# Kernel optimization log

Measured on AMD Instinct MI355X. Metric: run time of the kernel, lower is better.

The kernel has to match this reference:

```python
import jax, jax.numpy as jnp
import numpy as np

MAX_ITER = 3  # module default


def setup_inputs() -> dict:
    key = jax.random.key(0)
    k1, k2, k3 = jax.random.split(key, 3)
    B, S = 8, 160
    s_arc = jax.random.normal(k1, (B, S, S), dtype=jnp.float32)
    s_sib = jax.random.normal(k2, (B, S, S, S), dtype=jnp.float32)
    s_grd = jax.random.normal(k3, (B, S, S, S), dtype=jnp.float32)
    mask = jnp.ones((B, S), dtype=bool)
    return {"s_arc": s_arc, "s_sib": s_sib, "s_grd": s_grd, "mask": mask}


def reference(s_arc, s_sib, s_grd, mask):
    # Faithful batch-first rewrite of MFVIDependency.forward (target=None path).
    B, S = mask.shape
    m = mask.at[:, 0].set(True)  # index_fill: BOS/root position always valid
    idx = jnp.arange(S)
    # mask2o[b,h,d,s]: h,d,s all valid tokens AND s != h AND s != d
    # (torch builds hs=min(i,j), ms=max(i,j); excluding both == excluding h and d)
    m3 = m[:, :, None, None] & m[:, None, :, None] & m[:, None, None, :]
    neq = (idx[:, None, None] != idx[None, None, :]) & (idx[None, :, None] != idx[None, None, :])
    mask2o = m3 & neq[None]  # [B,S,S,S] = [b,h,d,s]

    # permute scores to [b, head, dep, (sib)] layout used inside the loop
    sib = jnp.transpose(s_sib, (0, 2, 1, 3)) * mask2o  # [b,h,d,s]
    grd = jnp.transpose(s_grd, (0, 2, 1, 3)) * mask2o  # [b,h,d,s]
    arc = jnp.transpose(s_arc, (0, 2, 1))              # [b,h,d]

    head_mask = m[:, :, None]  # [b,h,1] -> broadcast over dep dim
    q0 = jnp.broadcast_to(jnp.where(head_mask, 0.0, -jnp.inf), (B, S, S))

    def body(q, _):
        p = jax.nn.softmax(q, axis=1)  # normalize over heads
        f = (jnp.einsum('bhs,bhds->bhd', p, sib)
             + jnp.einsum('bds,bhds->bhd', p, grd))
        q_new = jnp.where(head_mask, arc + f, -jnp.inf)
        return q_new, None

    q, _ = jax.lax.scan(body, q0, None, length=MAX_ITER)
    # final: [b, dep, head] log-softmax over heads, then exp -> marginals
    logQ = jax.nn.log_softmax(jnp.transpose(q, (0, 2, 1)), axis=-1)
    return jnp.exp(logQ)
```

## Files before the change

### kernel.cpp

```cpp
#include <hip/hip_runtime.h>
#include <math.h>

#define Bn 8
#define Sn 160
#define BD (Bn * Sn)
#define BSS (Bn * Sn * Sn)
#define NCBLK (BD * 5)

typedef float f32x4 __attribute__((ext_vector_type(4)));
typedef unsigned short u16x8 __attribute__((ext_vector_type(8)));

__device__ __forceinline__ float bf2f(unsigned short u) {
    unsigned int x = ((unsigned int)u) << 16;
    return __builtin_bit_cast(float, x);
}
__device__ __forceinline__ unsigned short f2bf(float f) {
    unsigned int x = __builtin_bit_cast(unsigned int, f);
    x += 0x7fffu + ((x >> 16) & 1u);
    return (unsigned short)(x >> 16);
}

__global__ __launch_bounds__(256) void convert_fused_kernel(
    const float* __restrict__ sib, const float* __restrict__ grd,
    const float* __restrict__ arc,
    unsigned short* __restrict__ comb,
    float* __restrict__ qT)
{
    int bidx = blockIdx.x;
    int bd = bidx / 5;
    int o  = bidx - bd * 5;
    int d = bd % Sn;
    int w = threadIdx.x >> 6, lane = threadIdx.x & 63;
    int r = lane >> 3, sg = lane & 7;

    int h = o * 32 + w * 8 + r;
    size_t rb = ((size_t)bd * Sn + h) * Sn;
    const f32x4* srow = (const f32x4*)(sib + rb);
    const f32x4* grow = (const f32x4*)(grd + rb);

    float arcv = arc[(size_t)bd * Sn + h];

    f32x4 S[5], G[5];
    #pragma unroll
    for (int it = 0; it < 5; ++it) {
        int e4 = it * 8 + sg;
        S[it] = __builtin_nontemporal_load(srow + e4);
        G[it] = __builtin_nontemporal_load(grow + e4);
    }

    unsigned short* cb = comb + rb * 2;
    float acc = 0.f;
    #pragma unroll
    for (int it = 0; it < 5; ++it) {
        int e = it * 32 + sg * 4;
        u16x8 u;
        float vs, vg;
        int s;
        #pragma unroll
        for (int j = 0; j < 4; ++j) {
            s = e + j;
            if (s == h || s == d) { vs = 0.f; vg = 0.f; }
            else                  { vs = S[it][j]; vg = G[it][j]; }
            acc += vs + vg; u[j] = f2bf(vs); u[j + 4] = f2bf(vg);
        }
        *(u16x8*)(cb + (size_t)e * 2) = u;
    }
    acc += __shfl_xor(acc, 1, 64);
    acc += __shfl_xor(acc, 2, 64);
    acc += __shfl_xor(acc, 4, 64);
    if (sg == 0)
        qT[(size_t)bd * Sn + h] = arcv + acc * (1.0f / Sn);
}

__global__ __launch_bounds__(256) void softmax_p_kernel(
    const float* __restrict__ qT, float* __restrict__ p)
{
    int bd   = (blockIdx.x << 2) + (threadIdx.x >> 6);
    int lane = threadIdx.x & 63;
    int b = bd / Sn, d = bd % Sn;

    float4 v = make_float4(-INFINITY, -INFINITY, -INFINITY, -INFINITY);
    if (lane < 40) v = *(const float4*)(qT + (size_t)bd * Sn + lane * 4);

    float m = fmaxf(fmaxf(v.x, v.y), fmaxf(v.z, v.w));
    #pragma unroll
    for (int off = 32; off; off >>= 1)
        m = fmaxf(m, __shfl_xor(m, off, 64));

    float e0 = 0.f, e1 = 0.f, e2 = 0.f, e3 = 0.f;
    if (lane < 40) {
        e0 = expf(v.x - m); e1 = expf(v.y - m);
        e2 = expf(v.z - m); e3 = expf(v.w - m);
    }
    float ssum = e0 + e1 + e2 + e3;
    #pragma unroll
    for (int off = 32; off; off >>= 1)
        ssum += __shfl_xor(ssum, off, 64);
    float inv = 1.0f / ssum;

    if (lane < 40) {
        float* pb = p + (size_t)b * Sn * Sn + d;
        int h0 = lane * 4;
        pb[(size_t)(h0 + 0) * Sn] = e0 * inv;
        pb[(size_t)(h0 + 1) * Sn] = e1 * inv;
        pb[(size_t)(h0 + 2) * Sn] = e2 * inv;
        pb[(size_t)(h0 + 3) * Sn] = e3 * inv;
    }
}

template<int WRITE_OUT>
__global__ __launch_bounds__(256) void contract_sm_kernel(
    const unsigned short* __restrict__ comb,
    const float* __restrict__ arc, const float* __restrict__ p,
    float* __restrict__ outp)
{
    __shared__ float ls[Sn];

    int bd = blockIdx.x;
    int b = bd / Sn, d = bd % Sn;
    int w = threadIdx.x >> 6, lane = threadIdx.x & 63;
    int r = lane >> 3, sg = lane & 7;

    const float* pdp = p + ((size_t)b * Sn + d) * Sn;
    float4 pd4[5];
    #pragma unroll
    for (int it = 0; it < 5; ++it)
        pd4[it] = *(const float4*)(pdp + it * 32 + sg * 4);

    #pragma unroll
    for (int o = 0; o < 5; ++o) {
        int h = o * 32 + w * 8 + r;
        size_t rb = ((size_t)bd * Sn + h) * Sn;
        const u16x8* crow = (const u16x8*)(comb + rb * 2);
        const float* php = p + ((size_t)b * Sn + h) * Sn;

        u16x8 v[5];
        float4 ph4[5];
        #pragma unroll
        for (int it = 0; it < 5; ++it) {
            if (WRITE_OUT) v[it] = __builtin_nontemporal_load(crow + it * 8 + sg);
            else           v[it] = crow[it * 8 + sg];
            ph4[it] = *(const float4*)(php + it * 32 + sg * 4);
        }

        float acc = 0.f;
        #pragma unroll
        for (int it = 0; it < 5; ++it) {
            acc += bf2f(v[it][0]) * ph4[it].x + bf2f(v[it][4]) * pd4[it].x;
            acc += bf2f(v[it][1]) * ph4[it].y + bf2f(v[it][5]) * pd4[it].y;
            acc += bf2f(v[it][2]) * ph4[it].z + bf2f(v[it][6]) * pd4[it].z;
            acc += bf2f(v[it][3]) * ph4[it].w + bf2f(v[it][7]) * pd4[it].w;
        }
        acc += __shfl_xor(acc, 1, 64);
        acc += __shfl_xor(acc, 2, 64);
        acc += __shfl_xor(acc, 4, 64);
        if (sg == 0)
            ls[h] = arc[(size_t)bd * Sn + h] + acc;
    }

    __syncthreads();

    if (threadIdx.x < 64) {
        float4 v = make_float4(-INFINITY, -INFINITY, -INFINITY, -INFINITY);
        if (lane < 40) v = *(const float4*)(ls + lane * 4);

        float m = fmaxf(fmaxf(v.x, v.y), fmaxf(v.z, v.w));
        #pragma unroll
        for (int off = 32; off; off >>= 1)
            m = fmaxf(m, __shfl_xor(m, off, 64));

        float e0 = 0.f, e1 = 0.f, e2 = 0.f, e3 = 0.f;
        if (lane < 40) {
            e0 = expf(v.x - m); e1 = expf(v.y - m);
            e2 = expf(v.z - m); e3 = expf(v.w - m);
        }
        float ssum = e0 + e1 + e2 + e3;
        #pragma unroll
        for (int off = 32; off; off >>= 1)
            ssum += __shfl_xor(ssum, off, 64);
        float inv = 1.0f / ssum;

        if (lane < 40) {
            if (WRITE_OUT) {
                float4 rr = make_float4(e0 * inv, e1 * inv, e2 * inv, e3 * inv);
                *(float4*)(outp + (size_t)bd * Sn + lane * 4) = rr;
            } else {
                float* pb = outp + (size_t)b * Sn * Sn + d;
                int h0 = lane * 4;
                pb[(size_t)(h0 + 0) * Sn] = e0 * inv;
                pb[(size_t)(h0 + 1) * Sn] = e1 * inv;
                pb[(size_t)(h0 + 2) * Sn] = e2 * inv;
                pb[(size_t)(h0 + 3) * Sn] = e3 * inv;
            }
        }
    }
}

__global__ __launch_bounds__(256) void fill_p_kernel(float* __restrict__ p) {
    int i = blockIdx.x * 256 + threadIdx.x;
    p[i] = 1.0f / (float)Sn;
}

__global__ __launch_bounds__(256) void contract_f32_kernel(
    const float* __restrict__ sib, const float* __restrict__ grd,
    const float* __restrict__ arc, const float* __restrict__ p,
    float* __restrict__ qT)
{
    int bidx = blockIdx.x;
    int bd = bidx / 5;
    int o  = bidx - bd * 5;
    int b = bd / Sn, d = bd % Sn;
    int w = threadIdx.x >> 6, lane = threadIdx.x & 63;
    int r = lane >> 3, sg = lane & 7;

    int h = o * 32 + w * 8 + r;
    size_t rb = ((size_t)bd * Sn + h) * Sn;
    const f32x4* srow = (const f32x4*)(sib + rb);
    const f32x4* grow = (const f32x4*)(grd + rb);
    const f32x4* php  = (const f32x4*)(p + ((size_t)b * Sn + h) * Sn);
    const f32x4* pdp  = (const f32x4*)(p + ((size_t)b * Sn + d) * Sn);

    f32x4 S[5], G[5], PH[5], PD[5];
    #pragma unroll
    for (int it = 0; it < 5; ++it) {
        int e4 = it * 8 + sg;
        S[it]  = srow[e4];
        G[it]  = grow[e4];
        PH[it] = php[e4];
        PD[it] = pdp[e4];
    }

    float acc = 0.f;
    #pragma unroll
    for (int it = 0; it < 5; ++it) {
        int e = it * 32 + sg * 4;
        #pragma unroll
        for (int j = 0; j < 4; ++j) {
            int s = e + j;
            float t = S[it][j] * PH[it][j] + G[it][j] * PD[it][j];
            acc += (s != h && s != d) ? t : 0.f;
        }
    }
    acc += __shfl_xor(acc, 1, 64);
    acc += __shfl_xor(acc, 2, 64);
    acc += __shfl_xor(acc, 4, 64);
    if (sg == 0)
        qT[(size_t)bd * Sn + h] = arc[(size_t)bd * Sn + h] + acc;
}

__global__ __launch_bounds__(256) void softmax_out_kernel(
    const float* __restrict__ qT, float* __restrict__ out)
{
    int bd   = (blockIdx.x << 2) + (threadIdx.x >> 6);
    int lane = threadIdx.x & 63;

    float4 v = make_float4(-INFINITY, -INFINITY, -INFINITY, -INFINITY);
    if (lane < 40) v = *(const float4*)(qT + (size_t)bd * Sn + lane * 4);

    float m = fmaxf(fmaxf(v.x, v.y), fmaxf(v.z, v.w));
    #pragma unroll
    for (int off = 32; off; off >>= 1)
        m = fmaxf(m, __shfl_xor(m, off, 64));

    float e0 = 0.f, e1 = 0.f, e2 = 0.f, e3 = 0.f;
    if (lane < 40) {
        e0 = expf(v.x - m); e1 = expf(v.y - m);
        e2 = expf(v.z - m); e3 = expf(v.w - m);
    }
    float ssum = e0 + e1 + e2 + e3;
    #pragma unroll
    for (int off = 32; off; off >>= 1)
        ssum += __shfl_xor(ssum, off, 64);
    float inv = 1.0f / ssum;

    if (lane < 40) {
        float4 rr = make_float4(e0 * inv, e1 * inv, e2 * inv, e3 * inv);
        *(float4*)(out + (size_t)bd * Sn + lane * 4) = rr;
    }
}

extern "C" void kernel_launch(void* const* d_in, const int* in_sizes, int n_in,
                              void* d_out, int out_size, void* d_ws, size_t ws_size,
                              hipStream_t stream) {
    const float* s_arc = (const float*)d_in[0];
    const float* s_sib = (const float*)d_in[1];
    const float* s_grd = (const float*)d_in[2];
    float* out = (float*)d_out;

    const size_t comb_elems = 2 * (size_t)BSS * Sn;
    const size_t comb_bytes = comb_elems * 2;
    const size_t need       = comb_bytes + 2 * (size_t)BSS * 4;

    const int sm_blocks = BD / 4;

    if (ws_size >= need) {
        unsigned short* comb = (unsigned short*)d_ws;
        float* p  = (float*)((char*)d_ws + comb_bytes);
        float* qT = p + BSS;

        convert_fused_kernel<<<NCBLK, 256, 0, stream>>>(s_sib, s_grd, s_arc, comb, qT);
        softmax_p_kernel<<<sm_blocks, 256, 0, stream>>>(qT, p);
        contract_sm_kernel<0><<<BD, 256, 0, stream>>>(comb, s_arc, p, p);
        contract_sm_kernel<1><<<BD, 256, 0, stream>>>(comb, s_arc, p, out);
    } else {
        float* p  = (float*)d_ws;
        float* qT = p + BSS;
        fill_p_kernel<<<BSS / 256, 256, 0, stream>>>(p);
        contract_f32_kernel<<<NCBLK, 256, 0, stream>>>(s_sib, s_grd, s_arc, p, qT);
        softmax_p_kernel<<<sm_blocks, 256, 0, stream>>>(qT, p);
        contract_f32_kernel<<<NCBLK, 256, 0, stream>>>(s_sib, s_grd, s_arc, p, qT);
        softmax_p_kernel<<<sm_blocks, 256, 0, stream>>>(qT, p);
        contract_f32_kernel<<<NCBLK, 256, 0, stream>>>(s_sib, s_grd, s_arc, p, qT);
        softmax_out_kernel<<<sm_blocks, 256, 0, stream>>>(qT, out);
    }
}
```

Measured before the change: 114.6 us.

## Split fused pipeline into two batch halves to shrink working set

Runs the convert, softmax and two contraction kernels twice, each time over half of the (batch, dep) rows, using a new bd0 offset parameter. Each half covers whole batches, so per-batch dependencies between heads stay intact. The aim is to keep the bf16 combined-score buffer for a half resident in the last-level cache between the two contraction passes. In exchange it doubles the number of launches and halves each grid, which can worsen tail effects across CUs.

```diff
diff --git a/kernel.cpp b/kernel.cpp
--- a/kernel.cpp
+++ b/kernel.cpp
@@ -5,6 +5,8 @@
 #define Sn 160
 #define BD (Bn * Sn)
 #define BSS (Bn * Sn * Sn)
+#define BDH (BD / 2)
+#define NCBLK_H (BDH * 5)
 #define NCBLK (BD * 5)
 
 typedef float f32x4 __attribute__((ext_vector_type(4)));
@@ -24,11 +26,11 @@
     const float* __restrict__ sib, const float* __restrict__ grd,
     const float* __restrict__ arc,
     unsigned short* __restrict__ comb,
-    float* __restrict__ qT)
+    float* __restrict__ qT, int bd0)
 {
     int bidx = blockIdx.x;
-    int bd = bidx / 5;
-    int o  = bidx - bd * 5;
+    int bd = bd0 + bidx / 5;
+    int o  = bidx % 5;
     int d = bd % Sn;
     int w = threadIdx.x >> 6, lane = threadIdx.x & 63;
     int r = lane >> 3, sg = lane & 7;
@@ -73,9 +75,9 @@
 }
 
 __global__ __launch_bounds__(256) void softmax_p_kernel(
-    const float* __restrict__ qT, float* __restrict__ p)
-{
-    int bd   = (blockIdx.x << 2) + (threadIdx.x >> 6);
+    const float* __restrict__ qT, float* __restrict__ p, int bd0)
+{
+    int bd   = bd0 + (blockIdx.x << 2) + (threadIdx.x >> 6);
     int lane = threadIdx.x & 63;
     int b = bd / Sn, d = bd % Sn;
 
@@ -112,11 +114,11 @@
 __global__ __launch_bounds__(256) void contract_sm_kernel(
     const unsigned short* __restrict__ comb,
     const float* __restrict__ arc, const float* __restrict__ p,
-    float* __restrict__ outp)
+    float* __restrict__ outp, int bd0)
 {
     __shared__ float ls[Sn];
 
-    int bd = blockIdx.x;
+    int bd = bd0 + blockIdx.x;
     int b = bd / Sn, d = bd % Sn;
     int w = threadIdx.x >> 6, lane = threadIdx.x & 63;
     int r = lane >> 3, sg = lane & 7;
@@ -291,26 +293,29 @@
     const size_t comb_bytes = comb_elems * 2;
     const size_t need       = comb_bytes + 2 * (size_t)BSS * 4;
 
-    const int sm_blocks = BD / 4;
-
     if (ws_size >= need) {
         unsigned short* comb = (unsigned short*)d_ws;
         float* p  = (float*)((char*)d_ws + comb_bytes);
         float* qT = p + BSS;
 
-        convert_fused_kernel<<<NCBLK, 256, 0, stream>>>(s_sib, s_grd, s_arc, comb, qT);
-        softmax_p_kernel<<<sm_blocks, 256, 0, stream>>>(qT, p);
-        contract_sm_kernel<0><<<BD, 256, 0, stream>>>(comb, s_arc, p, p);
-        contract_sm_kernel<1><<<BD, 256, 0, stream>>>(comb, s_arc, p, out);
+        for (int half = 0; half < 2; ++half) {
+            int bd0 = half * BDH;
+            convert_fused_kernel<<<NCBLK_H, 256, 0, stream>>>(
+                s_sib, s_grd, s_arc, comb, qT, bd0);
+            softmax_p_kernel<<<BDH / 4, 256, 0, stream>>>(qT, p, bd0);
+            contract_sm_kernel<0><<<BDH, 256, 0, stream>>>(comb, s_arc, p, p, bd0);
+            contract_sm_kernel<1><<<BDH, 256, 0, stream>>>(comb, s_arc, p, out, bd0);
+        }
     } else {
         float* p  = (float*)d_ws;
         float* qT = p + BSS;
+        const int sm_blocks = BD / 4;
         fill_p_kernel<<<BSS / 256, 256, 0, stream>>>(p);
         contract_f32_kernel<<<NCBLK, 256, 0, stream>>>(s_sib, s_grd, s_arc, p, qT);
-        softmax_p_kernel<<<sm_blocks, 256, 0, stream>>>(qT, p);
+        softmax_p_kernel<<<sm_blocks, 256, 0, stream>>>(qT, p, 0);
         contract_f32_kernel<<<NCBLK, 256, 0, stream>>>(s_sib, s_grd, s_arc, p, qT);
-        softmax_p_kernel<<<sm_blocks, 256, 0, stream>>>(qT, p);
+        softmax_p_kernel<<<sm_blocks, 256, 0, stream>>>(qT, p, 0);
         contract_f32_kernel<<<NCBLK, 256, 0, stream>>>(s_sib, s_grd, s_arc, p, qT);
-        softmax_out_kernel<<<sm_blocks, 256, 0, stream>>>(qT, out);
-    }
-}
+        softmax_out_kernel<<<BD / 4, 256, 0, stream>>>(qT, out);
+    }
+}
```

Measured after the change: 122.2 us. 1.07x slower.
